# Kernel optimization log

Hardware: AMD Instinct MI355X
Metric: run time of the kernel (lower is better)

Reference implementation:

```python
import jax, jax.numpy as jnp
import numpy as np

L, D, V = 8, 1024, 32000
DT_MIN, DT_MAX = 0.01, 0.1
EPS = 1e-5


def _layer_norm(x, w, b):
    mu = jnp.mean(x, -1, keepdims=True)
    var = jnp.var(x, -1, keepdims=True)
    return (x - mu) * jax.lax.rsqrt(var + EPS) * w + b


def _encode(ids):
    # deterministic phase encoding of tokens onto the unit phase sphere
    theta = 2.0 * jnp.pi * ids.astype(jnp.float32) / V  # [B,S]
    k = jnp.arange(1, D // 2 + 1, dtype=jnp.float32)
    ang = theta[..., None] * k  # [B,S,D/2]
    return jnp.concatenate([jnp.cos(ang), jnp.sin(ang)], -1) / jnp.sqrt(jnp.float32(D))


def _flux(s, mask):
    # attention-like causal score from state self-interaction
    score = jnp.einsum('bqd,bkd->bqk', s, s) / jnp.sqrt(jnp.float32(D))
    score = jnp.where(mask, score, 0.0)
    return jnp.einsum('bqk,bkd->bqd', score, s), score


def _evolve_with_tunneling(s, dt, mask):
    # Heun-Euler (predictor-corrector) integration step
    k1, score = _flux(s, mask)
    mid = s + dt * k1
    k2, _ = _flux(mid, mask)
    ev = s + 0.5 * dt * (k1 + k2)
    # quantum tunneling: boost low-energy states proportionally to dt/dt_max
    energy = jnp.linalg.norm(ev, axis=-1)  # [B,S]
    thr = jnp.mean(energy, axis=-1, keepdims=True)
    tunnel = energy < thr
    strength = dt / DT_MAX  # [B,1,1]
    ev = jnp.where(tunnel[..., None], ev * (1.0 + strength), ev)
    ratio = jnp.mean(tunnel.astype(jnp.float32))
    return ev, score, ratio


def setup_inputs() -> dict:
    key = jax.random.key(0)
    ks = jax.random.split(key, 4)
    B, S = 2, 2048
    input_ids = jax.random.randint(ks[0], (B, S), 0, V)
    labels = jax.random.randint(ks[1], (B, S), 0, V)
    proj_w = jax.random.normal(ks[2], (L, D, D), jnp.float32) * 0.02
    proj_b = jnp.zeros((L, D), jnp.float32)
    ln_w = jnp.ones((L, D), jnp.float32)
    ln_b = jnp.zeros((L, D), jnp.float32)
    fln_w = jnp.ones((D,), jnp.float32)
    fln_b = jnp.zeros((D,), jnp.float32)
    out_w = jax.random.normal(ks[3], (D, V), jnp.float32) * 0.02
    return dict(input_ids=input_ids, labels=labels, proj_w=proj_w, proj_b=proj_b,
                ln_w=ln_w, ln_b=ln_b, fln_w=fln_w, fln_b=fln_b, out_w=out_w)


def reference(input_ids, labels, proj_w, proj_b, ln_w, ln_b, fln_w, fln_b, out_w):
    B, S = input_ids.shape
    mask = jnp.tril(jnp.ones((S, S), dtype=bool))
    # deterministic timestep (midpoint of [dt_min, dt_max]); dropout in eval mode
    dt = jnp.full((B, 1, 1), 0.5 * (DT_MIN + DT_MAX), jnp.float32)
    states = _encode(input_ids)
    for i in range(L):
        ev, _score, _ratio = _evolve_with_tunneling(states, dt, mask)
        states = _layer_norm(ev @ proj_w[i] + proj_b[i], ln_w[i], ln_b[i])
    states = _layer_norm(states, fln_w, fln_b)
    # normalized quantum projection to vocab
    energy = jnp.linalg.norm(states, axis=-1, keepdims=True)
    logits = (states / (energy + 1e-12)) @ out_w  # [B,S,V]
    # shifted cross-entropy
    sl = logits[:, :-1, :].reshape(-1, V)
    tl = labels[:, 1:].reshape(-1)
    logp = jax.nn.log_softmax(sl, axis=-1)
    loss = -jnp.mean(jnp.take_along_axis(logp, tl[:, None], axis=1))
    return logits, loss
```

## Files before the change

kernel.cpp:

```cpp
#include <hip/hip_runtime.h>

#define LL 8
#define DD 1024
#define VV 32000
#define SS 2048
#define BB 2
#define NROWS 4096
#define DT_STEP 0.055f
#define HALF_DT 0.0275f
#define TUNNEL_SCALE 1.55f

typedef __attribute__((ext_vector_type(8))) short bf16x8;
typedef __attribute__((ext_vector_type(4))) float f32x4;

static __device__ __forceinline__ float bf2f(unsigned short u){
  union { unsigned int i; float f; } v; v.i = ((unsigned int)u) << 16; return v.f;
}
static __device__ __forceinline__ unsigned short f2bf(float f){
  union { float f; unsigned int i; } v; v.f = f;
  unsigned int r = v.i + 0x7fffu + ((v.i >> 16) & 1u);
  return (unsigned short)(r >> 16);
}

static __device__ __forceinline__ void gl16(const unsigned short* g, unsigned short* l){
  __builtin_amdgcn_global_load_lds(
      (const __attribute__((address_space(1))) unsigned int*)g,
      (__attribute__((address_space(3))) unsigned int*)l, 16, 0, 0);
}

__device__ __forceinline__ float block_sum256(float v, volatile float* scratch){
  #pragma unroll
  for (int off = 32; off; off >>= 1) v += __shfl_down(v, off, 64);
  int w = threadIdx.x >> 6, lane = threadIdx.x & 63;
  __syncthreads();
  if (lane == 0) scratch[w] = v;
  __syncthreads();
  return scratch[0] + scratch[1] + scratch[2] + scratch[3];
}

__global__ void encode_kernel(const int* __restrict__ ids, float* __restrict__ s_f32,
                              unsigned short* __restrict__ hi, unsigned short* __restrict__ lo){
  int row = blockIdx.x;
  int t = threadIdx.x;
  float theta = 6.28318530717958647692f * (float)ids[row] / 32000.0f;
  #pragma unroll
  for (int i = 0; i < 2; ++i){
    int kk = t + i * 256;
    float ang = theta * (float)(kk + 1);
    float sv, cv; sincosf(ang, &sv, &cv);
    float c = cv * 0.03125f, s = sv * 0.03125f;
    long b0 = (long)row * DD + kk, b1 = b0 + 512;
    s_f32[b0] = c; s_f32[b1] = s;
    unsigned short ch = f2bf(c); hi[b0] = ch; lo[b0] = f2bf(c - bf2f(ch));
    unsigned short sh = f2bf(s); hi[b1] = sh; lo[b1] = f2bf(s - bf2f(sh));
  }
}

__global__ void transpose_bf16_pair_kernel(const unsigned short* __restrict__ in_hi,
                                           const unsigned short* __restrict__ in_lo,
                                           unsigned short* __restrict__ out_hi,
                                           unsigned short* __restrict__ out_lo,
                                           int R, int C){
  __shared__ __align__(16) unsigned short tile[64][80];
  int zz = blockIdx.z;
  const unsigned short* in = (zz & 1) ? in_lo : in_hi;
  unsigned short* out = (zz & 1) ? out_lo : out_hi;
  long ib = (long)(zz >> 1) * R * C;
  int c0 = blockIdx.x * 64, r0 = blockIdx.y * 64;
  int t = threadIdx.x;
  #pragma unroll
  for (int i = 0; i < 2; ++i){
    int j = t + i * 256; int row = j >> 3, cc = j & 7;
    *(uint4*)&tile[row][cc * 8] = *(const uint4*)(in + ib + (long)(r0 + row) * C + c0 + cc * 8);
  }
  __syncthreads();
  #pragma unroll
  for (int i = 0; i < 2; ++i){
    int j = t + i * 256; int orow = j >> 3, cc = j & 7;
    union { unsigned short u[8]; uint4 v; } tmp;
    #pragma unroll
    for (int e = 0; e < 8; ++e) tmp.u[e] = tile[cc * 8 + e][orow];
    *(uint4*)(out + ib + (long)(c0 + orow) * R + r0 + cc * 8) = tmp.v;
  }
}

template<bool SPLIT>
__global__ void transpose_f32_bf16_kernel(const float* __restrict__ in,
                                          unsigned short* __restrict__ ohi,
                                          unsigned short* __restrict__ olo, int R, int C){
  __shared__ float tile[64][68];
  long ib = (long)blockIdx.z * R * C;
  int c0 = blockIdx.x * 64, r0 = blockIdx.y * 64;
  int t = threadIdx.x;
  #pragma unroll
  for (int i = 0; i < 4; ++i){
    int j = t + i * 256; int row = j >> 4, cc = j & 15;
    *(float4*)&tile[row][cc * 4] = *(const float4*)(in + ib + (long)(r0 + row) * C + c0 + cc * 4);
  }
  __syncthreads();
  #pragma unroll
  for (int i = 0; i < 2; ++i){
    int j = t + i * 256; int orow = j >> 3, cc = j & 7;
    union { unsigned short u[8]; uint4 v; } th, tl;
    #pragma unroll
    for (int e = 0; e < 8; ++e){
      float v = tile[cc * 8 + e][orow];
      unsigned short h = f2bf(v); th.u[e] = h;
      if (SPLIT) tl.u[e] = f2bf(v - bf2f(h));
    }
    long ob = ib + (long)(c0 + orow) * R + r0 + cc * 8;
    *(uint4*)(ohi + ob) = th.v;
    if (SPLIT) *(uint4*)(olo + ob) = tl.v;
  }
}

template<int OUTMODE, int CAUSAL>
__global__ __launch_bounds__(512, 4)
void gemm_nt_kernel(const unsigned short* __restrict__ Ahi, const unsigned short* __restrict__ Alo,
                    const unsigned short* __restrict__ Bhi, const unsigned short* __restrict__ Blo,
                    float* __restrict__ C, unsigned short* __restrict__ Chi,
                    unsigned short* __restrict__ Clo, const float* __restrict__ bias,
                    const float* __restrict__ Sf, const float* __restrict__ K1f,
                    int K, int lda, int ldb, int ldc, int MT, int NT,
                    long batchA, long batchB, long batchC, float alpha)
{
  const int bz = blockIdx.y;
  const int nwg = MT * NT;
  const int q = nwg >> 3, r = nwg & 7;
  const int xcd = blockIdx.x & 7, off = blockIdx.x >> 3;
  const int wg = (xcd < r ? xcd * (q + 1) : r * (q + 1) + (xcd - r) * q) + off;
  const int band = wg / (NT << 3), rem = wg - band * (NT << 3);
  const int mt = (band << 3) + (rem & 7), nt = rem >> 3;
  if (CAUSAL == 1 && nt > mt) return;
  const int m0 = mt << 7, n0 = nt << 7;
  int Keff = K;
  if (CAUSAL == 2){ int kl = (mt + 1) << 7; Keff = kl < K ? kl : K; }

  __shared__ __align__(16) unsigned short sA[2][128][64];
  __shared__ __align__(16) unsigned short sB[2][128][64];

  const int tid = threadIdx.x;
  const int lane = tid & 63;
  const int w = tid >> 6;
  const int wr = w >> 2, wc = w & 3;
  const int fr = lane & 15, fc = lane >> 4;
  const int fr7 = fr & 7;

  f32x4 acc[4][2];
  #pragma unroll
  for (int i = 0; i < 4; ++i)
    #pragma unroll
    for (int j = 0; j < 2; ++j) acc[i][j] = (f32x4){0.f, 0.f, 0.f, 0.f};

  const int srow = tid >> 3, slot = tid & 7;
  const int cont = slot ^ (srow & 7);
  const long aoff = (long)bz * batchA, boff = (long)bz * batchB;
  const int gcol = (cont & 3) << 3;
  const unsigned short* gA = (cont >= 4 ? Alo : Ahi) + aoff + (long)(m0 + srow) * lda + gcol;
  const unsigned short* gB = (cont >= 4 ? Blo : Bhi) + boff + (long)(n0 + srow) * ldb + gcol;
  const long rstepA = 64L * lda, rstepB = 64L * ldb;
  const int wofs = w << 9;

  #define STAGE(buf, kt) do {                                        \
    gl16(gA + (kt),          &sA[buf][0][0] + wofs);                 \
    gl16(gA + (kt) + rstepA, &sA[buf][0][0] + 4096 + wofs);          \
    gl16(gB + (kt),          &sB[buf][0][0] + wofs);                 \
    gl16(gB + (kt) + rstepB, &sB[buf][0][0] + 4096 + wofs);          \
  } while(0)

  const int oh = (fc ^ fr7) << 4;
  const int ol = ((4 + fc) ^ fr7) << 4;

  #define COMPUTE(buf) do {                                                         \
    const char* bA_ = (const char*)&sA[buf][0][0];                                  \
    const char* bB_ = (const char*)&sB[buf][0][0];                                  \
    bf16x8 ah_[4], al_[4];                                                          \
    _Pragma("unroll")                                                               \
    for (int mi = 0; mi < 4; ++mi){                                                 \
      const char* p_ = bA_ + (wr * 64 + mi * 16 + fr) * 128;                        \
      ah_[mi] = *(const bf16x8*)(p_ + oh);                                          \
      al_[mi] = *(const bf16x8*)(p_ + ol);                                          \
    }                                                                               \
    _Pragma("unroll")                                                               \
    for (int ni = 0; ni < 2; ++ni){                                                 \
      const char* pb_ = bB_ + (wc * 32 + ni * 16 + fr) * 128;                       \
      bf16x8 bh_ = *(const bf16x8*)(pb_ + oh);                                      \
      bf16x8 bl_ = *(const bf16x8*)(pb_ + ol);                                      \
      _Pragma("unroll")                                                             \
      for (int mi = 0; mi < 4; ++mi){                                               \
        acc[mi][ni] = __builtin_amdgcn_mfma_f32_16x16x32_bf16(ah_[mi], bh_, acc[mi][ni], 0, 0, 0);\
        acc[mi][ni] = __builtin_amdgcn_mfma_f32_16x16x32_bf16(ah_[mi], bl_, acc[mi][ni], 0, 0, 0);\
        acc[mi][ni] = __builtin_amdgcn_mfma_f32_16x16x32_bf16(al_[mi], bh_, acc[mi][ni], 0, 0, 0);\
      }                                                                             \
    }                                                                               \
  } while(0)

  const int ntiles = Keff >> 5;

  STAGE(0, 0);
  int cur = 0;
  for (int t = 0; t < ntiles - 1; ++t){
    asm volatile("s_barrier" ::: "memory");
    STAGE(cur ^ 1, (t + 1) << 5);
    asm volatile("s_waitcnt vmcnt(4)" ::: "memory");
    asm volatile("s_barrier" ::: "memory");
    COMPUTE(cur);
    cur ^= 1;
  }
  asm volatile("s_waitcnt vmcnt(0)" ::: "memory");
  asm volatile("s_barrier" ::: "memory");
  COMPUTE(cur);

  #undef STAGE
  #undef COMPUTE

  const long coff = (long)bz * batchC;
  const int rb0 = m0 + wr * 64 + fc * 4;
  const int cb0 = n0 + wc * 32 + fr;
  #pragma unroll
  for (int mi = 0; mi < 4; ++mi){
    #pragma unroll
    for (int ni = 0; ni < 2; ++ni){
      #pragma unroll
      for (int rg = 0; rg < 4; ++rg){
        int row = rb0 + mi * 16 + rg;
        int col = cb0 + ni * 16;
        float v = acc[mi][ni][rg] * alpha;
        long idx = coff + (long)row * ldc + col;
        if (OUTMODE == 0){
          if (bias) v += bias[col];
          C[idx] = v;
        } else if (OUTMODE == 2){
          if (CAUSAL == 1 && col > row) v = 0.0f;
          unsigned short h = f2bf(v);
          Chi[idx] = h;
          Clo[idx] = f2bf(v - bf2f(h));
        } else if (OUTMODE == 3){
          C[idx] = v;
          float m = Sf[idx] + DT_STEP * v;
          unsigned short h = f2bf(m);
          Chi[idx] = h;
          Clo[idx] = f2bf(m - bf2f(h));
        } else {
          C[idx] = Sf[idx] + HALF_DT * (K1f[idx] + v);
        }
      }
    }
  }
}

__global__ __launch_bounds__(512, 2)
void gemm256_kernel(const unsigned short* __restrict__ A,
                    const unsigned short* __restrict__ Bt,
                    float* __restrict__ C)
{
  const int MT = 16, NT = 125;
  const int nwg = MT * NT;
  const int q = nwg >> 3, r = nwg & 7;
  const int xcd = blockIdx.x & 7, off = blockIdx.x >> 3;
  const int wg = (xcd < r ? xcd * (q + 1) : r * (q + 1) + (xcd - r) * q) + off;
  const int band = wg / (NT << 3), rem = wg - band * (NT << 3);
  const int mt = (band << 3) + (rem & 7), nt = rem >> 3;
  const int m0 = mt << 8, n0 = nt << 8;

  __shared__ __align__(16) unsigned short sA[2][256][64];
  __shared__ __align__(16) unsigned short sB[2][256][64];

  const int tid = threadIdx.x;
  const int lane = tid & 63;
  const int w = tid >> 6;
  const int wr = w >> 2, wc = w & 3;
  const int fr = lane & 15, fc = lane >> 4;
  const int fr7 = fr & 7;

  f32x4 acc[8][4];
  #pragma unroll
  for (int i = 0; i < 8; ++i)
    #pragma unroll
    for (int j = 0; j < 4; ++j) acc[i][j] = (f32x4){0.f, 0.f, 0.f, 0.f};

  const int srow = tid >> 3, slot = tid & 7;
  const int cont = slot ^ (srow & 7);
  const unsigned short* gA = A  + (long)(m0 + srow) * DD + (cont << 3);
  const unsigned short* gB = Bt + (long)(n0 + srow) * DD + (cont << 3);
  const int wofs = w << 9;

  #define SGA(buf, kt, i) gl16(gA + (long)((i) * 64) * DD + (kt), &sA[buf][0][0] + (i) * 4096 + wofs)
  #define SGB(buf, kt, i) gl16(gB + (long)((i) * 64) * DD + (kt), &sB[buf][0][0] + (i) * 4096 + wofs)

  const int oh = (fc ^ fr7) << 4;
  const int ol = ((4 + fc) ^ fr7) << 4;

  #pragma unroll
  for (int i = 0; i < 4; ++i){ SGA(0, 0, i); SGB(0, 0, i); }

  int cur = 0;
  for (int t = 0; t < 16; ++t){
    const int nk = (t + 1) << 6;
    const bool stg = (t < 15);
    const char* bA = (const char*)&sA[cur][0][0];
    const char* bB = (const char*)&sB[cur][0][0];
    bf16x8 aq[4][2], bq[4][2];

    if (stg){ SGA(cur ^ 1, nk, 0); SGA(cur ^ 1, nk, 1);
              asm volatile("s_waitcnt vmcnt(2)" ::: "memory"); }
    else    { asm volatile("s_waitcnt vmcnt(0)" ::: "memory"); }
    asm volatile("s_barrier" ::: "memory");
    #pragma unroll
    for (int mi = 0; mi < 4; ++mi){
      const char* p = bA + (wr * 128 + mi * 16 + fr) * 128;
      aq[mi][0] = *(const bf16x8*)(p + oh);
      aq[mi][1] = *(const bf16x8*)(p + ol);
    }
    #pragma unroll
    for (int ni = 0; ni < 2; ++ni){
      const char* p = bB + (wc * 64 + ni * 16 + fr) * 128;
      bq[ni][0] = *(const bf16x8*)(p + oh);
      bq[ni][1] = *(const bf16x8*)(p + ol);
    }
    __builtin_amdgcn_s_setprio(1);
    #pragma unroll
    for (int ks = 0; ks < 2; ++ks)
      #pragma unroll
      for (int mi = 0; mi < 4; ++mi)
        #pragma unroll
        for (int ni = 0; ni < 2; ++ni)
          acc[mi][ni] = __builtin_amdgcn_mfma_f32_16x16x32_bf16(aq[mi][ks], bq[ni][ks], acc[mi][ni], 0, 0, 0);
    __builtin_amdgcn_s_setprio(0);

    if (stg){ SGA(cur ^ 1, nk, 2); SGA(cur ^ 1, nk, 3); }
    asm volatile("s_barrier" ::: "memory");
    #pragma unroll
    for (int ni = 2; ni < 4; ++ni){
      const char* p = bB + (wc * 64 + ni * 16 + fr) * 128;
      bq[ni][0] = *(const bf16x8*)(p + oh);
      bq[ni][1] = *(const bf16x8*)(p + ol);
    }
    __builtin_amdgcn_s_setprio(1);
    #pragma unroll
    for (int ks = 0; ks < 2; ++ks)
      #pragma unroll
      for (int mi = 0; mi < 4; ++mi)
        #pragma unroll
        for (int ni = 2; ni < 4; ++ni)
          acc[mi][ni] = __builtin_amdgcn_mfma_f32_16x16x32_bf16(aq[mi][ks], bq[ni][ks], acc[mi][ni], 0, 0, 0);
    __builtin_amdgcn_s_setprio(0);

    if (stg){ SGB(cur ^ 1, nk, 0); SGB(cur ^ 1, nk, 1); }
    asm volatile("s_barrier" ::: "memory");
    #pragma unroll
    for (int mi = 0; mi < 4; ++mi){
      const char* p = bA + (wr * 128 + (mi + 4) * 16 + fr) * 128;
      aq[mi][0] = *(const bf16x8*)(p + oh);
      aq[mi][1] = *(const bf16x8*)(p + ol);
    }
    __builtin_amdgcn_s_setprio(1);
    #pragma unroll
    for (int ks = 0; ks < 2; ++ks)
      #pragma unroll
      for (int mi = 0; mi < 4; ++mi)
        #pragma unroll
        for (int ni = 2; ni < 4; ++ni)
          acc[mi + 4][ni] = __builtin_amdgcn_mfma_f32_16x16x32_bf16(aq[mi][ks], bq[ni][ks], acc[mi + 4][ni], 0, 0, 0);
    __builtin_amdgcn_s_setprio(0);

    if (stg){ SGB(cur ^ 1, nk, 2); SGB(cur ^ 1, nk, 3); }
    asm volatile("s_barrier" ::: "memory");
    __builtin_amdgcn_s_setprio(1);
    #pragma unroll
    for (int ks = 0; ks < 2; ++ks)
      #pragma unroll
      for (int mi = 0; mi < 4; ++mi)
        #pragma unroll
        for (int ni = 0; ni < 2; ++ni)
          acc[mi + 4][ni] = __builtin_amdgcn_mfma_f32_16x16x32_bf16(aq[mi][ks], bq[ni][ks], acc[mi + 4][ni], 0, 0, 0);
    __builtin_amdgcn_s_setprio(0);

    cur ^= 1;
  }
  #undef SGA
  #undef SGB

  const int rb0 = m0 + wr * 128 + fc * 4;
  const int cb0 = n0 + wc * 64 + fr;
  #pragma unroll
  for (int mi = 0; mi < 8; ++mi){
    #pragma unroll
    for (int ni = 0; ni < 4; ++ni){
      #pragma unroll
      for (int rg = 0; rg < 4; ++rg){
        int row = rb0 + mi * 16 + rg;
        int col = cb0 + ni * 16;
        C[(long)row * VV + col] = acc[mi][ni][rg];
      }
    }
  }
}

__global__ void energy_kernel(const float* __restrict__ ev, float* __restrict__ energy){
  int row = blockIdx.x, t = threadIdx.x;
  long base = (long)row * DD + t * 4;
  float4 v = *(const float4*)(ev + base);
  __shared__ float scratch[4];
  float n2 = block_sum256(v.x*v.x + v.y*v.y + v.z*v.z + v.w*v.w, scratch);
  if (t == 0) energy[row] = sqrtf(n2);
}

__global__ void mean_energy_kernel(const float* __restrict__ energy, float* __restrict__ thr){
  int b = blockIdx.x, t = threadIdx.x;
  float s = 0.f;
  for (int j = t; j < SS; j += 256) s += energy[b * SS + j];
  __shared__ float scratch[4];
  float tot = block_sum256(s, scratch);
  if (t == 0) thr[b] = tot * (1.0f / SS);
}

__global__ void tunnel_kernel(const float* __restrict__ ev, const float* __restrict__ energy,
                              const float* __restrict__ thr,
                              unsigned short* __restrict__ hi, unsigned short* __restrict__ lo){
  int row = blockIdx.x, t = threadIdx.x;
  float scale = (energy[row] < thr[row >> 11]) ? TUNNEL_SCALE : 1.0f;
  long base = (long)row * DD + t * 4;
  float4 v = *(const float4*)(ev + base);
  v.x *= scale; v.y *= scale; v.z *= scale; v.w *= scale;
  ushort4 hv, lv;
  hv.x = f2bf(v.x); lv.x = f2bf(v.x - bf2f(hv.x));
  hv.y = f2bf(v.y); lv.y = f2bf(v.y - bf2f(hv.y));
  hv.z = f2bf(v.z); lv.z = f2bf(v.z - bf2f(hv.z));
  hv.w = f2bf(v.w); lv.w = f2bf(v.w - bf2f(hv.w));
  *(ushort4*)(hi + base) = hv; *(ushort4*)(lo + base) = lv;
}

__global__ void ln_kernel(const float* __restrict__ h, const float* __restrict__ w,
                          const float* __restrict__ b, float* __restrict__ s_f32,
                          unsigned short* __restrict__ hi, unsigned short* __restrict__ lo){
  int row = blockIdx.x, t = threadIdx.x;
  long base = (long)row * DD + t * 4;
  float4 xv = *(const float4*)(h + base);
  __shared__ float scratch[4];
  float sum = block_sum256(xv.x + xv.y + xv.z + xv.w, scratch);
  float ssq = block_sum256(xv.x*xv.x + xv.y*xv.y + xv.z*xv.z + xv.w*xv.w, scratch);
  float mu = sum * (1.0f / DD);
  float var = ssq * (1.0f / DD) - mu * mu;
  float rstd = rsqrtf(var + 1e-5f);
  float4 wv = *(const float4*)(w + t * 4), bv = *(const float4*)(b + t * 4);
  float y0 = (xv.x - mu) * rstd * wv.x + bv.x;
  float y1 = (xv.y - mu) * rstd * wv.y + bv.y;
  float y2 = (xv.z - mu) * rstd * wv.z + bv.z;
  float y3 = (xv.w - mu) * rstd * wv.w + bv.w;
  float4 o; o.x = y0; o.y = y1; o.z = y2; o.w = y3;
  *(float4*)(s_f32 + base) = o;
  ushort4 hv, lv;
  hv.x = f2bf(y0); lv.x = f2bf(y0 - bf2f(hv.x));
  hv.y = f2bf(y1); lv.y = f2bf(y1 - bf2f(hv.y));
  hv.z = f2bf(y2); lv.z = f2bf(y2 - bf2f(hv.z));
  hv.w = f2bf(y3); lv.w = f2bf(y3 - bf2f(hv.w));
  *(ushort4*)(hi + base) = hv; *(ushort4*)(lo + base) = lv;
}

__global__ void fln_kernel(const float* __restrict__ s, const float* __restrict__ w,
                           const float* __restrict__ b, unsigned short* __restrict__ uhi){
  int row = blockIdx.x, t = threadIdx.x;
  long base = (long)row * DD + t * 4;
  float4 xv = *(const float4*)(s + base);
  __shared__ float scratch[4];
  float sum = block_sum256(xv.x + xv.y + xv.z + xv.w, scratch);
  float ssq = block_sum256(xv.x*xv.x + xv.y*xv.y + xv.z*xv.z + xv.w*xv.w, scratch);
  float mu = sum * (1.0f / DD);
  float var = ssq * (1.0f / DD) - mu * mu;
  float rstd = rsqrtf(var + 1e-5f);
  float4 wv = *(const float4*)(w + t * 4), bv = *(const float4*)(b + t * 4);
  float y0 = (xv.x - mu) * rstd * wv.x + bv.x;
  float y1 = (xv.y - mu) * rstd * wv.y + bv.y;
  float y2 = (xv.z - mu) * rstd * wv.z + bv.z;
  float y3 = (xv.w - mu) * rstd * wv.w + bv.w;
  float n2 = block_sum256(y0*y0 + y1*y1 + y2*y2 + y3*y3, scratch);
  float inv = 1.0f / (sqrtf(n2) + 1e-12f);
  ushort4 o;
  o.x = f2bf(y0 * inv); o.y = f2bf(y1 * inv);
  o.z = f2bf(y2 * inv); o.w = f2bf(y3 * inv);
  *(ushort4*)(uhi + base) = o;
}

__global__ void loss_rows_kernel(const float* __restrict__ logits, const int* __restrict__ labels,
                                 float* __restrict__ lrow){
  int idx = blockIdx.x;
  int b = idx / (SS - 1), q = idx - b * (SS - 1);
  const float* rowp = logits + (long)(b * SS + q) * VV;
  int t = threadIdx.x;
  float m = -1e30f, l = 0.f;
  for (int j = t; j < VV / 4; j += 256){
    float4 v = *(const float4*)(rowp + j * 4);
    float mv = fmaxf(fmaxf(v.x, v.y), fmaxf(v.z, v.w));
    if (mv > m){ l *= __expf(m - mv); m = mv; }
    l += __expf(v.x - m) + __expf(v.y - m) + __expf(v.z - m) + __expf(v.w - m);
  }
  __shared__ float sm[256], sl[256];
  sm[t] = m; sl[t] = l;
  __syncthreads();
  for (int off = 128; off; off >>= 1){
    if (t < off){
      float m2 = sm[t + off], l2 = sl[t + off];
      float M = fmaxf(sm[t], m2);
      sl[t] = sl[t] * __expf(sm[t] - M) + l2 * __expf(m2 - M);
      sm[t] = M;
    }
    __syncthreads();
  }
  if (t == 0){
    float lse = sm[0] + __logf(sl[0]);
    float tl = rowp[labels[b * SS + q + 1]];
    lrow[idx] = lse - tl;
  }
}

__global__ void loss_reduce_kernel(const float* __restrict__ lrow, float* __restrict__ dst){
  __shared__ float scratch[4];
  float s = 0.f;
  for (int j = threadIdx.x; j < BB * (SS - 1); j += 256) s += lrow[j];
  float tot = block_sum256(s, scratch);
  if (threadIdx.x == 0) dst[0] = tot / (float)(BB * (SS - 1));
}

extern "C" void kernel_launch(void* const* d_in, const int* in_sizes, int n_in,
                              void* d_out, int out_size, void* d_ws, size_t ws_size,
                              hipStream_t stream) {
  const int*   ids    = (const int*)d_in[0];
  const int*   labels = (const int*)d_in[1];
  const float* proj_w = (const float*)d_in[2];
  const float* proj_b = (const float*)d_in[3];
  const float* ln_w   = (const float*)d_in[4];
  const float* ln_b   = (const float*)d_in[5];
  const float* fln_w  = (const float*)d_in[6];
  const float* fln_b  = (const float*)d_in[7];
  const float* out_w  = (const float*)d_in[8];
  float* out = (float*)d_out;

  char* ws = (char*)d_ws;
  float*          s_f32 = (float*)(ws + 0);
  unsigned short* op_hi = (unsigned short*)(ws + 16777216);
  unsigned short* op_lo = (unsigned short*)(ws + 25165824);
  unsigned short* T_hi  = (unsigned short*)(ws + 33554432);
  unsigned short* T_lo  = (unsigned short*)(ws + 41943040);
  float*          k1    = (float*)(ws + 50331648);
  float*          k2    = (float*)(ws + 67108864);
  unsigned short* sc_hi = (unsigned short*)(ws + 83886080);
  unsigned short* sc_lo = (unsigned short*)(ws + 92274688);
  unsigned short* WhiT  = (unsigned short*)(ws + 100663296);
  unsigned short* WloT  = (unsigned short*)(ws + 117440512);
  float*          energy= (float*)(ws + 134217728);
  float*          thr   = (float*)(ws + 134234112);
  float*          lrow  = (float*)(ws + 134234368);
  unsigned short* owT   = T_hi;

  transpose_f32_bf16_kernel<true><<<dim3(16, 16, 8), 256, 0, stream>>>(proj_w, WhiT, WloT, DD, DD);
  encode_kernel<<<NROWS, 256, 0, stream>>>(ids, s_f32, op_hi, op_lo);
  transpose_bf16_pair_kernel<<<dim3(16, 32, 4), 256, 0, stream>>>(op_hi, op_lo, T_hi, T_lo, SS, DD);

  for (int l = 0; l < LL; ++l){
    gemm_nt_kernel<2, 1><<<dim3(256, 2), 512, 0, stream>>>(
        op_hi, op_lo, op_hi, op_lo, nullptr, sc_hi, sc_lo, nullptr, nullptr, nullptr,
        DD, DD, DD, SS, 16, 16, (long)SS * DD, (long)SS * DD, (long)SS * SS, 0.03125f);
    gemm_nt_kernel<3, 2><<<dim3(128, 2), 512, 0, stream>>>(
        sc_hi, sc_lo, T_hi, T_lo, k1, op_hi, op_lo, nullptr, s_f32, nullptr,
        SS, SS, SS, DD, 16, 8, (long)SS * SS, (long)DD * SS, (long)SS * DD, 1.0f);
    transpose_bf16_pair_kernel<<<dim3(16, 32, 4), 256, 0, stream>>>(op_hi, op_lo, T_hi, T_lo, SS, DD);
    gemm_nt_kernel<2, 1><<<dim3(256, 2), 512, 0, stream>>>(
        op_hi, op_lo, op_hi, op_lo, nullptr, sc_hi, sc_lo, nullptr, nullptr, nullptr,
        DD, DD, DD, SS, 16, 16, (long)SS * DD, (long)SS * DD, (long)SS * SS, 0.03125f);
    gemm_nt_kernel<4, 2><<<dim3(128, 2), 512, 0, stream>>>(
        sc_hi, sc_lo, T_hi, T_lo, k2, nullptr, nullptr, nullptr, s_f32, k1,
        SS, SS, SS, DD, 16, 8, (long)SS * SS, (long)DD * SS, (long)SS * DD, 1.0f);
    energy_kernel<<<NROWS, 256, 0, stream>>>(k2, energy);
    mean_energy_kernel<<<BB, 256, 0, stream>>>(energy, thr);
    tunnel_kernel<<<NROWS, 256, 0, stream>>>(k2, energy, thr, op_hi, op_lo);
    gemm_nt_kernel<0, 0><<<dim3(256, 1), 512, 0, stream>>>(
        op_hi, op_lo, WhiT + (long)l * DD * DD, WloT + (long)l * DD * DD,
        k1, nullptr, nullptr, proj_b + l * DD, nullptr, nullptr,
        DD, DD, DD, DD, 32, 8, 0, 0, 0, 1.0f);
    ln_kernel<<<NROWS, 256, 0, stream>>>(k1, ln_w + l * DD, ln_b + l * DD, s_f32, op_hi, op_lo);
    if (l < LL - 1){
      transpose_bf16_pair_kernel<<<dim3(16, 32, 4), 256, 0, stream>>>(op_hi, op_lo, T_hi, T_lo, SS, DD);
    }
  }

  transpose_f32_bf16_kernel<false><<<dim3(500, 16, 1), 256, 0, stream>>>(out_w, owT, nullptr, DD, VV);
  fln_kernel<<<NROWS, 256, 0, stream>>>(s_f32, fln_w, fln_b, op_hi);
  gemm256_kernel<<<2000, 512, 0, stream>>>(op_hi, owT, out);
  loss_rows_kernel<<<BB * (SS - 1), 256, 0, stream>>>(out, labels, lrow);
  loss_reduce_kernel<<<1, 256, 0, stream>>>(lrow, out + (long)NROWS * VV);
}
```

Measured before the change: 3.000 ms.

## Shrink gemm_nt tiles to 128x64 and fuse softmax partials into vocab GEMM

The split-bf16 GEMM drops from 512 threads with 128x128 tiles to 256 threads with 128x64 tiles. Grid sizes and NT are doubled to match, which gives more workgroups and finer causal skipping. Separately, the vocab GEMM epilogue now computes per-row partial max and sum-exp for each 64-column chunk, so the loss kernel merges 500 partials per row instead of rereading the full 32000-wide logits row. The partials reuse the workspace region of s_f32, which is dead by then. The trade-offs are extra shuffles and exp work in the GEMM epilogue, and lower per-block reuse in gemm_nt.

```diff
diff --git a/kernel.cpp b/kernel.cpp
--- a/kernel.cpp
+++ b/kernel.cpp
@@ -115,7 +115,7 @@
 }
 
 template<int OUTMODE, int CAUSAL>
-__global__ __launch_bounds__(512, 4)
+__global__ __launch_bounds__(256, 3)
 void gemm_nt_kernel(const unsigned short* __restrict__ Ahi, const unsigned short* __restrict__ Alo,
                     const unsigned short* __restrict__ Bhi, const unsigned short* __restrict__ Blo,
                     float* __restrict__ C, unsigned short* __restrict__ Chi,
@@ -131,18 +131,18 @@
   const int wg = (xcd < r ? xcd * (q + 1) : r * (q + 1) + (xcd - r) * q) + off;
   const int band = wg / (NT << 3), rem = wg - band * (NT << 3);
   const int mt = (band << 3) + (rem & 7), nt = rem >> 3;
-  if (CAUSAL == 1 && nt > mt) return;
-  const int m0 = mt << 7, n0 = nt << 7;
+  const int m0 = mt << 7, n0 = nt << 6;
+  if (CAUSAL == 1 && n0 > m0 + 127) return;
   int Keff = K;
   if (CAUSAL == 2){ int kl = (mt + 1) << 7; Keff = kl < K ? kl : K; }
 
   __shared__ __align__(16) unsigned short sA[2][128][64];
-  __shared__ __align__(16) unsigned short sB[2][128][64];
+  __shared__ __align__(16) unsigned short sB[2][64][64];
 
   const int tid = threadIdx.x;
   const int lane = tid & 63;
   const int w = tid >> 6;
-  const int wr = w >> 2, wc = w & 3;
+  const int wr = w >> 1, wc = w & 1;
   const int fr = lane & 15, fc = lane >> 4;
   const int fr7 = fr & 7;
 
@@ -158,14 +158,15 @@
   const int gcol = (cont & 3) << 3;
   const unsigned short* gA = (cont >= 4 ? Alo : Ahi) + aoff + (long)(m0 + srow) * lda + gcol;
   const unsigned short* gB = (cont >= 4 ? Blo : Bhi) + boff + (long)(n0 + srow) * ldb + gcol;
-  const long rstepA = 64L * lda, rstepB = 64L * ldb;
   const int wofs = w << 9;
 
-  #define STAGE(buf, kt) do {                                        \
-    gl16(gA + (kt),          &sA[buf][0][0] + wofs);                 \
-    gl16(gA + (kt) + rstepA, &sA[buf][0][0] + 4096 + wofs);          \
-    gl16(gB + (kt),          &sB[buf][0][0] + wofs);                 \
-    gl16(gB + (kt) + rstepB, &sB[buf][0][0] + 4096 + wofs);          \
+  #define STAGE(buf, kt) do {                                            \
+    _Pragma("unroll")                                                    \
+    for (int i_ = 0; i_ < 4; ++i_)                                       \
+      gl16(gA + (kt) + (long)(i_ * 32) * lda, &sA[buf][0][0] + i_ * 2048 + wofs); \
+    _Pragma("unroll")                                                    \
+    for (int i_ = 0; i_ < 2; ++i_)                                       \
+      gl16(gB + (kt) + (long)(i_ * 32) * ldb, &sB[buf][0][0] + i_ * 2048 + wofs); \
   } while(0)
 
   const int oh = (fc ^ fr7) << 4;
@@ -202,7 +203,7 @@
   for (int t = 0; t < ntiles - 1; ++t){
     asm volatile("s_barrier" ::: "memory");
     STAGE(cur ^ 1, (t + 1) << 5);
-    asm volatile("s_waitcnt vmcnt(4)" ::: "memory");
+    asm volatile("s_waitcnt vmcnt(6)" ::: "memory");
     asm volatile("s_barrier" ::: "memory");
     COMPUTE(cur);
     cur ^= 1;
@@ -252,7 +253,9 @@
 __global__ __launch_bounds__(512, 2)
 void gemm256_kernel(const unsigned short* __restrict__ A,
                     const unsigned short* __restrict__ Bt,
-                    float* __restrict__ C)
+                    float* __restrict__ C,
+                    float* __restrict__ pmax,
+                    float* __restrict__ psum)
 {
   const int MT = 16, NT = 125;
   const int nwg = MT * NT;
@@ -389,9 +392,27 @@
     for (int ni = 0; ni < 4; ++ni){
       #pragma unroll
       for (int rg = 0; rg < 4; ++rg){
-        int row = rb0 + mi * 16 + rg;
-        int col = cb0 + ni * 16;
-        C[(long)row * VV + col] = acc[mi][ni][rg];
+        C[(long)(rb0 + mi * 16 + rg) * VV + cb0 + ni * 16] = acc[mi][ni][rg];
+      }
+    }
+  }
+
+  #pragma unroll
+  for (int mi = 0; mi < 8; ++mi){
+    #pragma unroll
+    for (int rg = 0; rg < 4; ++rg){
+      float m4 = fmaxf(fmaxf(acc[mi][0][rg], acc[mi][1][rg]),
+                       fmaxf(acc[mi][2][rg], acc[mi][3][rg]));
+      #pragma unroll
+      for (int o = 1; o < 16; o <<= 1) m4 = fmaxf(m4, __shfl_xor(m4, o, 64));
+      float s4 = __expf(acc[mi][0][rg] - m4) + __expf(acc[mi][1][rg] - m4)
+               + __expf(acc[mi][2][rg] - m4) + __expf(acc[mi][3][rg] - m4);
+      #pragma unroll
+      for (int o = 1; o < 16; o <<= 1) s4 += __shfl_xor(s4, o, 64);
+      if (fr == 0){
+        long pidx = ((long)(rb0 + mi * 16 + rg) << 9) + nt * 4 + wc;
+        pmax[pidx] = m4;
+        psum[pidx] = s4;
       }
     }
   }
@@ -482,34 +503,30 @@
   *(ushort4*)(uhi + base) = o;
 }
 
-__global__ void loss_rows_kernel(const float* __restrict__ logits, const int* __restrict__ labels,
-                                 float* __restrict__ lrow){
+__global__ void lse_reduce_kernel(const float* __restrict__ pmax, const float* __restrict__ psum,
+                                  const float* __restrict__ logits, const int* __restrict__ labels,
+                                  float* __restrict__ lrow){
   int idx = blockIdx.x;
-  int b = idx / (SS - 1), q = idx - b * (SS - 1);
-  const float* rowp = logits + (long)(b * SS + q) * VV;
+  int b = idx / (SS - 1), qq = idx - b * (SS - 1);
+  int row = b * SS + qq;
   int t = threadIdx.x;
   float m = -1e30f, l = 0.f;
-  for (int j = t; j < VV / 4; j += 256){
-    float4 v = *(const float4*)(rowp + j * 4);
-    float mv = fmaxf(fmaxf(v.x, v.y), fmaxf(v.z, v.w));
-    if (mv > m){ l *= __expf(m - mv); m = mv; }
-    l += __expf(v.x - m) + __expf(v.y - m) + __expf(v.z - m) + __expf(v.w - m);
-  }
-  __shared__ float sm[256], sl[256];
-  sm[t] = m; sl[t] = l;
-  __syncthreads();
-  for (int off = 128; off; off >>= 1){
-    if (t < off){
-      float m2 = sm[t + off], l2 = sl[t + off];
-      float M = fmaxf(sm[t], m2);
-      sl[t] = sl[t] * __expf(sm[t] - M) + l2 * __expf(m2 - M);
-      sm[t] = M;
-    }
-    __syncthreads();
+  for (int p = t; p < 500; p += 64){
+    float pm = pmax[((long)row << 9) + p], pl = psum[((long)row << 9) + p];
+    float M = fmaxf(m, pm);
+    l = l * __expf(m - M) + pl * __expf(pm - M);
+    m = M;
+  }
+  #pragma unroll
+  for (int o = 1; o < 64; o <<= 1){
+    float m2 = __shfl_xor(m, o, 64), l2 = __shfl_xor(l, o, 64);
+    float M = fmaxf(m, m2);
+    l = l * __expf(m - M) + l2 * __expf(m2 - M);
+    m = M;
   }
   if (t == 0){
-    float lse = sm[0] + __logf(sl[0]);
-    float tl = rowp[labels[b * SS + q + 1]];
+    float lse = m + __logf(l);
+    float tl = logits[(long)row * VV + labels[row + 1]];
     lrow[idx] = lse - tl;
   }
 }
@@ -552,32 +569,34 @@
   float*          thr   = (float*)(ws + 134234112);
   float*          lrow  = (float*)(ws + 134234368);
   unsigned short* owT   = T_hi;
+  float*          pmax  = (float*)(ws + 0);
+  float*          psum  = (float*)(ws + 8388608);
 
   transpose_f32_bf16_kernel<true><<<dim3(16, 16, 8), 256, 0, stream>>>(proj_w, WhiT, WloT, DD, DD);
   encode_kernel<<<NROWS, 256, 0, stream>>>(ids, s_f32, op_hi, op_lo);
   transpose_bf16_pair_kernel<<<dim3(16, 32, 4), 256, 0, stream>>>(op_hi, op_lo, T_hi, T_lo, SS, DD);
 
   for (int l = 0; l < LL; ++l){
-    gemm_nt_kernel<2, 1><<<dim3(256, 2), 512, 0, stream>>>(
+    gemm_nt_kernel<2, 1><<<dim3(512, 2), 256, 0, stream>>>(
         op_hi, op_lo, op_hi, op_lo, nullptr, sc_hi, sc_lo, nullptr, nullptr, nullptr,
-        DD, DD, DD, SS, 16, 16, (long)SS * DD, (long)SS * DD, (long)SS * SS, 0.03125f);
-    gemm_nt_kernel<3, 2><<<dim3(128, 2), 512, 0, stream>>>(
+        DD, DD, DD, SS, 16, 32, (long)SS * DD, (long)SS * DD, (long)SS * SS, 0.03125f);
+    gemm_nt_kernel<3, 2><<<dim3(256, 2), 256, 0, stream>>>(
         sc_hi, sc_lo, T_hi, T_lo, k1, op_hi, op_lo, nullptr, s_f32, nullptr,
-        SS, SS, SS, DD, 16, 8, (long)SS * SS, (long)DD * SS, (long)SS * DD, 1.0f);
+        SS, SS, SS, DD, 16, 16, (long)SS * SS, (long)DD * SS, (long)SS * DD, 1.0f);
     transpose_bf16_pair_kernel<<<dim3(16, 32, 4), 256, 0, stream>>>(op_hi, op_lo, T_hi, T_lo, SS, DD);
-    gemm_nt_kernel<2, 1><<<dim3(256, 2), 512, 0, stream>>>(
+    gemm_nt_kernel<2, 1><<<dim3(512, 2), 256, 0, stream>>>(
         op_hi, op_lo, op_hi, op_lo, nullptr, sc_hi, sc_lo, nullptr, nullptr, nullptr,
-        DD, DD, DD, SS, 16, 16, (long)SS * DD, (long)SS * DD, (long)SS * SS, 0.03125f);
-    gemm_nt_kernel<4, 2><<<dim3(128, 2), 512, 0, stream>>>(
+        DD, DD, DD, SS, 16, 32, (long)SS * DD, (long)SS * DD, (long)SS * SS, 0.03125f);
+    gemm_nt_kernel<4, 2><<<dim3(256, 2), 256, 0, stream>>>(
         sc_hi, sc_lo, T_hi, T_lo, k2, nullptr, nullptr, nullptr, s_f32, k1,
-        SS, SS, SS, DD, 16, 8, (long)SS * SS, (long)DD * SS, (long)SS * DD, 1.0f);
+        SS, SS, SS, DD, 16, 16, (long)SS * SS, (long)DD * SS, (long)SS * DD, 1.0f);
     energy_kernel<<<NROWS, 256, 0, stream>>>(k2, energy);
     mean_energy_kernel<<<BB, 256, 0, stream>>>(energy, thr);
     tunnel_kernel<<<NROWS, 256, 0, stream>>>(k2, energy, thr, op_hi, op_lo);
-    gemm_nt_kernel<0, 0><<<dim3(256, 1), 512, 0, stream>>>(
+    gemm_nt_kernel<0, 0><<<dim3(512, 1), 256, 0, stream>>>(
         op_hi, op_lo, WhiT + (long)l * DD * DD, WloT + (long)l * DD * DD,
         k1, nullptr, nullptr, proj_b + l * DD, nullptr, nullptr,
-        DD, DD, DD, DD, 32, 8, 0, 0, 0, 1.0f);
+        DD, DD, DD, DD, 32, 16, 0, 0, 0, 1.0f);
     ln_kernel<<<NROWS, 256, 0, stream>>>(k1, ln_w + l * DD, ln_b + l * DD, s_f32, op_hi, op_lo);
     if (l < LL - 1){
       transpose_bf16_pair_kernel<<<dim3(16, 32, 4), 256, 0, stream>>>(op_hi, op_lo, T_hi, T_lo, SS, DD);
@@ -586,7 +605,7 @@
 
   transpose_f32_bf16_kernel<false><<<dim3(500, 16, 1), 256, 0, stream>>>(out_w, owT, nullptr, DD, VV);
   fln_kernel<<<NROWS, 256, 0, stream>>>(s_f32, fln_w, fln_b, op_hi);
-  gemm256_kernel<<<2000, 512, 0, stream>>>(op_hi, owT, out);
-  loss_rows_kernel<<<BB * (SS - 1), 256, 0, stream>>>(out, labels, lrow);
+  gemm256_kernel<<<2000, 512, 0, stream>>>(op_hi, owT, out, pmax, psum);
+  lse_reduce_kernel<<<BB * (SS - 1), 64, 0, stream>>>(pmax, psum, out, labels, lrow);
   loss_reduce_kernel<<<1, 256, 0, stream>>>(lrow, out + (long)NROWS * VV);
 }
```

Result: slower. 3.233 ms (+7.7%).
